# Optimization experiments

Measured on AMD Instinct MI355X. Metric: run time of the kernel, lower is better.

Reference implementation:

```python
import jax, jax.numpy as jnp
import numpy as np

B, L, D, H, DK, DV = 2, 2048, 512, 8, 64, 64
EPS = 1e-6


def setup_inputs() -> dict:
    key = jax.random.key(0)
    ks = jax.random.split(key, 19)
    n = lambda k, s: jax.random.normal(k, s, dtype=jnp.float32)
    inp = {
        "q_r": n(ks[0], (B, L, D)), "q_i": n(ks[1], (B, L, D)),
        "k_r": n(ks[2], (B, L, D)), "k_i": n(ks[3], (B, L, D)),
        "v_r": n(ks[4], (B, L, D)), "v_i": n(ks[5], (B, L, D)),
        "wq_r": n(ks[6], (D, H * DK)) * 0.02, "wq_i": n(ks[7], (D, H * DK)) * 0.02,
        "wk_r": n(ks[8], (D, H * DK)) * 0.02, "wk_i": n(ks[9], (D, H * DK)) * 0.02,
        "wv_r": n(ks[10], (D, H * DV)) * 0.02, "wv_i": n(ks[11], (D, H * DV)) * 0.02,
        "wo_r": n(ks[12], (H * DV, D)) * 0.02, "wo_i": n(ks[13], (H * DV, D)) * 0.02,
        "ln_wr": n(ks[14], (D,)), "ln_wi": n(ks[15], (D,)),
        "ln_br": n(ks[16], (D,)), "ln_bi": n(ks[17], (D,)),
        "mask": jax.random.randint(ks[18], (B, L, L), 0, 2).astype(jnp.int32),
    }
    return inp


def _clinear(xr, xi, wr, wi):
    # complex matmul (xr + i xi) @ (wr + i wi)
    return xr @ wr - xi @ wi, xi @ wr + xr @ wi


def _complex_layernorm(r, i, wr, wi, br, bi, eps=EPS):
    axes = (1, 2)  # normalize over all non-batch dims of [B, L, D]
    r = r - r.mean(axis=axes, keepdims=True)
    i = i - i.mean(axis=axes, keepdims=True)
    Crr = (r * r).mean(axis=axes, keepdims=True) + eps
    Cii = (i * i).mean(axis=axes, keepdims=True) + eps
    Cri = (r * i).mean(axis=axes, keepdims=True)
    s = jnp.sqrt(Crr * Cii - Cri * Cri)
    t = jnp.sqrt(Crr + Cii + 2.0 * s)
    inv_st = 1.0 / (s * t)
    Rrr = (Cii + s) * inv_st
    Rii = (Crr + s) * inv_st
    Rri = -Cri * inv_st
    nr = Rrr * r + Rri * i
    ni = Rii * i + Rri * r
    # affine: complex multiply by (wr + i wi), then add complex bias
    out_r = nr * wr - ni * wi + br
    out_i = nr * wi + ni * wr + bi
    return out_r, out_i


def reference(q_r, q_i, k_r, k_i, v_r, v_i,
              wq_r, wq_i, wk_r, wk_i, wv_r, wv_i, wo_r, wo_i,
              ln_wr, ln_wi, ln_br, ln_bi, mask):
    res_r, res_i = q_r, q_i
    qr, qi = _clinear(q_r, q_i, wq_r, wq_i)
    kr, ki = _clinear(k_r, k_i, wk_r, wk_i)
    vr, vi = _clinear(v_r, v_i, wv_r, wv_i)
    # [B, L, H*Dk] -> [B, H, L, Dk]
    tohead = lambda x, d: x.reshape(B, L, H, d).transpose(0, 2, 1, 3)
    qr, qi = tohead(qr, DK), tohead(qi, DK)
    kr, ki = tohead(kr, DK), tohead(ki, DK)
    vr, vi = tohead(vr, DV), tohead(vi, DV)
    temp = jnp.float32(DK) ** 0.5
    qr, qi = qr / temp, qi / temp
    # complex scores (q @ conj(k)^T): re + i*im
    sr = jnp.einsum('bhqd,bhkd->bhqk', qr, kr) + jnp.einsum('bhqd,bhkd->bhqk', qi, ki)
    si = jnp.einsum('bhqd,bhkd->bhqk', qi, kr) - jnp.einsum('bhqd,bhkd->bhqk', qr, ki)
    a = jnp.sqrt(sr * sr + si * si)  # abs of complex scores
    a = jnp.where(mask[:, None, :, :] == 0, jnp.float32(-1e9), a)
    attn = jax.nn.softmax(a, axis=-1)  # real-valued attention weights
    out_r = jnp.einsum('bhqk,bhkd->bhqd', attn, vr)
    out_i = jnp.einsum('bhqk,bhkd->bhqd', attn, vi)
    # [B, H, L, Dv] -> [B, L, H*Dv]
    out_r = out_r.transpose(0, 2, 1, 3).reshape(B, L, H * DV)
    out_i = out_i.transpose(0, 2, 1, 3).reshape(B, L, H * DV)
    out_r, out_i = _clinear(out_r, out_i, wo_r, wo_i)
    out_r = out_r + res_r
    out_i = out_i + res_i
    out_r, out_i = _complex_layernorm(out_r, out_i, ln_wr, ln_wi, ln_br, ln_bi)
    return out_r, out_i, attn
```

## Files before the change

kernel.cpp:

```cpp
#include <hip/hip_runtime.h>

typedef unsigned short u16;
typedef unsigned int u32;
typedef unsigned long long u64;


typedef __attribute__((ext_vector_type(8))) short bf16x8;
typedef __attribute__((ext_vector_type(4))) float f32x4;
typedef __attribute__((ext_vector_type(4))) u32 u32x4;

__device__ __forceinline__ u16 f2bf(float f) {
  u32 x = __float_as_uint(f);
  return (u16)((x + 0x7FFFu + ((x >> 16) & 1u)) >> 16);
}
__device__ __forceinline__ u32 pk2(float a, float b) {
  return (u32)f2bf(a) | ((u32)f2bf(b) << 16);
}
__device__ __forceinline__ bf16x8 negv(bf16x8 v) {
  u32x4 x = __builtin_bit_cast(u32x4, v);
  x ^= 0x80008000u;
  return __builtin_bit_cast(bf16x8, x);
}


__global__ __launch_bounds__(256) void pack_a3(
    const float* __restrict__ qr, const float* __restrict__ qi,
    const float* __restrict__ kr, const float* __restrict__ ki,
    const float* __restrict__ vr, const float* __restrict__ vi,
    u16* __restrict__ A) {
  int z = blockIdx.y;
  const float* r  = (z == 0) ? qr : (z == 1) ? kr : vr;
  const float* im = (z == 0) ? qi : (z == 1) ? ki : vi;
  int c = blockIdx.x * 256 + threadIdx.x;
  int m = c >> 7;
  int ck = (c & 127) * 8;
  const float* s = (ck < 512) ? (r + (size_t)m * 512 + ck)
                              : (im + (size_t)m * 512 + (ck - 512));
  float4 a = ((const float4*)s)[0];
  float4 b = ((const float4*)s)[1];
  uint4 o;
  o.x = pk2(a.x, a.y); o.y = pk2(a.z, a.w);
  o.z = pk2(b.x, b.y); o.w = pk2(b.z, b.w);
  ((uint4*)(A + (size_t)z * 4194304))[c] = o;
}

__global__ __launch_bounds__(256) void pack_bt(
    const float* __restrict__ wqr, const float* __restrict__ wqi,
    const float* __restrict__ wkr, const float* __restrict__ wki,
    const float* __restrict__ wvr, const float* __restrict__ wvi,
    const float* __restrict__ wor, const float* __restrict__ woi,
    u16* __restrict__ Btb) {
  int z = blockIdx.y;
  const float* wr = (z==0)?wqr:(z==1)?wkr:(z==2)?wvr:wor;
  const float* wi = (z==0)?wqi:(z==1)?wki:(z==2)?wvi:woi;
  u16* Bt = Btb + (size_t)z * 1048576;
  int n0 = (blockIdx.x >> 4) * 64;
  int k0 = (blockIdx.x & 15) * 64;
  __shared__ float tile[64][65];
  int t = threadIdx.x;
  bool nlow = (n0 < 512), klow = (k0 < 512);
  const float* src = nlow ? (klow ? wr : wi) : (klow ? wi : wr);
  float sgn = (nlow && !klow) ? -1.0f : 1.0f;
  int col0 = nlow ? n0 : n0 - 512;
  int kr0 = klow ? k0 : k0 - 512;
  {
    int rr = t >> 2, cc = (t & 3) * 16;
    const float4* s = (const float4*)(src + (size_t)(kr0 + rr) * 512 + col0 + cc);
#pragma unroll
    for (int j = 0; j < 4; ++j) {
      float4 v = s[j];
      tile[rr][cc + j*4 + 0] = v.x; tile[rr][cc + j*4 + 1] = v.y;
      tile[rr][cc + j*4 + 2] = v.z; tile[rr][cc + j*4 + 3] = v.w;
    }
  }
  __syncthreads();
  {
    int nn = t >> 2, kc = (t & 3) * 16;
    u32 w[8];
#pragma unroll
    for (int j = 0; j < 8; ++j)
      w[j] = pk2(sgn * tile[kc + 2*j][nn], sgn * tile[kc + 2*j + 1][nn]);
    uint4* d = (uint4*)(Bt + (size_t)(n0 + nn) * 1024 + k0 + kc);
    d[0] = make_uint4(w[0], w[1], w[2], w[3]);
    d[1] = make_uint4(w[4], w[5], w[6], w[7]);
  }
}

__global__ __launch_bounds__(256) void pack_mask(const int* __restrict__ mask,
                                                 u64* __restrict__ mb) {
  int tid = blockIdx.x * 256 + threadIdx.x;
  u64 bal = __ballot(mask[tid] != 0);
  if ((threadIdx.x & 63) == 0) mb[tid >> 6] = bal;
}

__global__ __launch_bounds__(256) void pack_vt(const u16* __restrict__ Cvm,
                                               u16* __restrict__ vt) {
  int z = blockIdx.y;
  int b = z >> 3, h = z & 7;
  int lt = blockIdx.x >> 1, ct = blockIdx.x & 1;
  int l0 = lt * 64, c0 = ct * 64;
  int n0 = (ct == 0) ? (h * 64) : (512 + h * 64);
  __shared__ u16 tile[64][80];
  int t = threadIdx.x;
  {
    int lr = t >> 2, cc = (t & 3) * 16;
    const uint4* s = (const uint4*)(Cvm + ((size_t)(b * 2048 + l0 + lr)) * 1024 + n0 + cc);
    uint4 v0 = s[0], v1 = s[1];
    *(uint4*)&tile[lr][cc] = v0;
    *(uint4*)&tile[lr][cc + 8] = v1;
  }
  __syncthreads();
  {
    int cr = t >> 2, lc = (t & 3) * 16;
    u32 w[8];
#pragma unroll
    for (int j = 0; j < 8; ++j)
      w[j] = (u32)tile[lc + 2*j][cr] | ((u32)tile[lc + 2*j + 1][cr] << 16);
    uint4* d = (uint4*)(vt + ((size_t)z * 128 + c0 + cr) * 2048 + l0 + lc);
    d[0] = make_uint4(w[0], w[1], w[2], w[3]);
    d[1] = make_uint4(w[4], w[5], w[6], w[7]);
  }
}


__device__ __forceinline__ void stage_bf(const u16* __restrict__ g, int ld,
                                         u16* lds, int t) {
#pragma unroll
  for (int p = 0; p < 4; ++p) {
    int id = p * 256 + t;
    int r = id >> 3, c = id & 7;
    uint4 v = *(const uint4*)(g + (size_t)r * ld + c * 8);
    *(uint4*)(lds + r * 64 + ((c ^ (r & 7)) << 3)) = v;
  }
}
__device__ __forceinline__ void stage64(const u16* __restrict__ g, int ld,
                                        u16* lds, int t) {
#pragma unroll
  for (int p = 0; p < 2; ++p) {
    int id = p * 256 + t;
    int r = id >> 3, c = id & 7;
    uint4 v = *(const uint4*)(g + (size_t)r * ld + c * 8);
    *(uint4*)(lds + r * 64 + ((c ^ (r & 7)) << 3)) = v;
  }
}

__global__ __launch_bounds__(256) void gemm_proj(const u16* __restrict__ Abase,
                                                 const u16* __restrict__ Btbase,
                                                 u16* __restrict__ Cbase) {
  __shared__ u16 lA[128 * 64], lB[128 * 64];
  int t = threadIdx.x, lane = t & 63, wid = t >> 6;
  int c15 = lane & 15, g = lane >> 4, l7 = lane & 7;
  int z = blockIdx.z;
  const u16* A  = Abase  + (size_t)z * 4194304;
  const u16* Bt = Btbase + (size_t)z * 1048576;
  u16* C = Cbase + (size_t)z * 4194304;
  int brow = blockIdx.y * 128, bcol = blockIdx.x * 128;
  float scale = (z == 0) ? 0.125f : 1.0f;
  int sw0 = ((g ^ l7) << 3), sw1 = (((4 | g) ^ l7) << 3);
  int wr0 = (wid >> 1) * 64 + c15, wc0 = (wid & 1) * 64 + c15;
  const u16 *pA0 = lA + wr0 * 64 + sw0, *pA1 = lA + wr0 * 64 + sw1;
  const u16 *pB0 = lB + wc0 * 64 + sw0, *pB1 = lB + wc0 * 64 + sw1;
  f32x4 zero = {0.f, 0.f, 0.f, 0.f};
  f32x4 acc[4][4];
#pragma unroll
  for (int mi = 0; mi < 4; ++mi)
#pragma unroll
    for (int ni = 0; ni < 4; ++ni) acc[mi][ni] = zero;
  for (int kt = 0; kt < 1024; kt += 64) {
    stage_bf(A + (size_t)brow * 1024 + kt, 1024, lA, t);
    stage_bf(Bt + (size_t)bcol * 1024 + kt, 1024, lB, t);
    __syncthreads();
#pragma unroll
    for (int ks = 0; ks < 2; ++ks) {
      const u16* pa = ks ? pA1 : pA0;
      const u16* pb = ks ? pB1 : pB0;
      bf16x8 fa[4], fb[4];
#pragma unroll
      for (int i2 = 0; i2 < 4; ++i2) {
        fa[i2] = *(const bf16x8*)(pa + i2 * 1024);
        fb[i2] = *(const bf16x8*)(pb + i2 * 1024);
      }
#pragma unroll
      for (int mi = 0; mi < 4; ++mi)
#pragma unroll
        for (int ni = 0; ni < 4; ++ni)
          acc[mi][ni] = __builtin_amdgcn_mfma_f32_16x16x32_bf16(
              fa[mi], fb[ni], acc[mi][ni], 0, 0, 0);
    }
    __syncthreads();
  }
  int wrb = (wid >> 1) * 64, wcb = (wid & 1) * 64;
  int rj = g * 4, cj = c15;
#pragma unroll
  for (int mi = 0; mi < 4; ++mi)
#pragma unroll
    for (int ni = 0; ni < 4; ++ni)
#pragma unroll
      for (int j = 0; j < 4; ++j)
        C[(size_t)(brow + wrb + mi * 16 + rj + j) * 1024 +
          (bcol + wcb + ni * 16 + cj)] = f2bf(acc[mi][ni][j] * scale);
}

__global__ __launch_bounds__(256, 3) void fused_attn(
    const u16* __restrict__ Cq, const u16* __restrict__ Ck,
    const u16* __restrict__ vt, const u64* __restrict__ mb,
    float* __restrict__ attn, u16* __restrict__ Ao) {
  __shared__ u16 lKr[64 * 64], lKi[64 * 64], lV[128 * 64], lP[64 * 64];
  int t = threadIdx.x, lane = t & 63, w = t >> 6;
  int c15 = lane & 15, g = lane >> 4, l7 = lane & 7;
  int f = blockIdx.x + (int)gridDim.x * blockIdx.y;
  int wk = (f & 7) * 64 + (f >> 3);
  int strip = wk & 31, z = wk >> 5;
  int b = z >> 3, h = z & 7;
  int q0 = strip * 64;
  int arow = w * 16 + c15;
  int rbase = w * 16 + (g << 2);

  const u16* Qrow = Cq + ((size_t)(b * 2048 + q0 + arow)) * 1024 + h * 64;
  bf16x8 q0r = *(const bf16x8*)(Qrow + g * 8);
  bf16x8 q1r = *(const bf16x8*)(Qrow + 32 + g * 8);
  bf16x8 q0i = *(const bf16x8*)(Qrow + 512 + g * 8);
  bf16x8 q1i = *(const bf16x8*)(Qrow + 544 + g * 8);
  bf16x8 nq0r = negv(q0r), nq1r = negv(q1r);

  int sw0 = ((g ^ l7) << 3), sw1 = (((4 | g) ^ l7) << 3);
  const u16 *pKr0 = lKr + c15 * 64 + sw0, *pKr1 = lKr + c15 * 64 + sw1;
  const u16 *pKi0 = lKi + c15 * 64 + sw0, *pKi1 = lKi + c15 * 64 + sw1;
  const u16 *pV0 = lV + c15 * 64 + sw0, *pV1 = lV + c15 * 64 + sw1;
  const u16 *pP0 = lP + arow * 64 + sw0, *pP1 = lP + arow * 64 + sw1;

  size_t mbase = ((size_t)(b * 2048 + q0 + rbase)) * 32;
  float s[4] = {0.f, 0.f, 0.f, 0.f};
  f32x4 zero = {0.f, 0.f, 0.f, 0.f};
  f32x4 o[8];
#pragma unroll
  for (int ni = 0; ni < 8; ++ni) o[ni] = zero;

  const u16* Kb = Ck + ((size_t)(b * 2048)) * 1024 + h * 64;
  const u16* Vb = vt + (size_t)z * 262144;

  for (int tl = 0; tl < 32; ++tl) {
    int l0 = tl * 64;
    if (tl) __syncthreads();
    stage64(Kb + (size_t)l0 * 1024, 1024, lKr, t);
    stage64(Kb + (size_t)l0 * 1024 + 512, 1024, lKi, t);
    stage_bf(Vb + l0, 2048, lV, t);
    __syncthreads();
    f32x4 sr[4], si[4];
#pragma unroll
    for (int ni = 0; ni < 4; ++ni) { sr[ni] = zero; si[ni] = zero; }
#pragma unroll
    for (int ni = 0; ni < 4; ++ni) {
      bf16x8 g0 = *(const bf16x8*)(pKr0 + ni * 1024);
      bf16x8 g1 = *(const bf16x8*)(pKi0 + ni * 1024);
      sr[ni] = __builtin_amdgcn_mfma_f32_16x16x32_bf16(q0r, g0, sr[ni], 0, 0, 0);
      sr[ni] = __builtin_amdgcn_mfma_f32_16x16x32_bf16(q0i, g1, sr[ni], 0, 0, 0);
      si[ni] = __builtin_amdgcn_mfma_f32_16x16x32_bf16(q0i, g0, si[ni], 0, 0, 0);
      si[ni] = __builtin_amdgcn_mfma_f32_16x16x32_bf16(nq0r, g1, si[ni], 0, 0, 0);
      bf16x8 h0 = *(const bf16x8*)(pKr1 + ni * 1024);
      bf16x8 h1 = *(const bf16x8*)(pKi1 + ni * 1024);
      sr[ni] = __builtin_amdgcn_mfma_f32_16x16x32_bf16(q1r, h0, sr[ni], 0, 0, 0);
      sr[ni] = __builtin_amdgcn_mfma_f32_16x16x32_bf16(q1i, h1, sr[ni], 0, 0, 0);
      si[ni] = __builtin_amdgcn_mfma_f32_16x16x32_bf16(q1i, h0, si[ni], 0, 0, 0);
      si[ni] = __builtin_amdgcn_mfma_f32_16x16x32_bf16(nq1r, h1, si[ni], 0, 0, 0);
    }
    u64 wm[4];
#pragma unroll
    for (int j = 0; j < 4; ++j) wm[j] = mb[mbase + (size_t)j * 32 + tl];
#pragma unroll
    for (int ni = 0; ni < 4; ++ni) {
      int cbit = ni * 16 + c15;
      int pchi = ni * 2 + (c15 >> 3);
#pragma unroll
      for (int j = 0; j < 4; ++j) {
        float n = sr[ni][j] * sr[ni][j] + si[ni][j] * si[ni][j];
        float p = __expf(__builtin_amdgcn_sqrtf(n));
        p = ((wm[j] >> cbit) & 1ull) ? p : 0.0f;
        s[j] += p;
        lP[(rbase + j) * 64 + ((pchi ^ (((g & 1) << 2) + j)) << 3) + l7] = f2bf(p);
      }
    }
    {
      bf16x8 fa0 = *(const bf16x8*)pP0;
      bf16x8 fa1 = *(const bf16x8*)pP1;
#pragma unroll
      for (int ni = 0; ni < 8; ++ni) {
        bf16x8 fb0 = *(const bf16x8*)(pV0 + ni * 1024);
        bf16x8 fb1 = *(const bf16x8*)(pV1 + ni * 1024);
        o[ni] = __builtin_amdgcn_mfma_f32_16x16x32_bf16(fa0, fb0, o[ni], 0, 0, 0);
        o[ni] = __builtin_amdgcn_mfma_f32_16x16x32_bf16(fa1, fb1, o[ni], 0, 0, 0);
      }
    }
  }
  float inv[4];
#pragma unroll
  for (int j = 0; j < 4; ++j) {
    float sj = s[j];
#pragma unroll
    for (int off = 1; off < 16; off <<= 1) sj += __shfl_xor(sj, off);
    inv[j] = 1.0f / sj;
  }
#pragma unroll
  for (int ni = 0; ni < 8; ++ni) {
    int c = ni * 16 + c15;
    int nout = (c < 64) ? (h * 64 + c) : (512 + h * 64 + (c - 64));
#pragma unroll
    for (int j = 0; j < 4; ++j)
      Ao[((size_t)(b * 2048 + q0 + rbase + j)) * 1024 + nout] =
          f2bf(o[ni][j] * inv[j]);
  }
  float* arow_out = attn + ((size_t)z * 2048 + q0 + rbase) * 2048 + c15;
  for (int tl = 0; tl < 32; ++tl) {
    int l0 = tl * 64;
    __syncthreads();
    stage64(Kb + (size_t)l0 * 1024, 1024, lKr, t);
    stage64(Kb + (size_t)l0 * 1024 + 512, 1024, lKi, t);
    __syncthreads();
    f32x4 sr[4], si[4];
#pragma unroll
    for (int ni = 0; ni < 4; ++ni) { sr[ni] = zero; si[ni] = zero; }
#pragma unroll
    for (int ni = 0; ni < 4; ++ni) {
      bf16x8 g0 = *(const bf16x8*)(pKr0 + ni * 1024);
      bf16x8 g1 = *(const bf16x8*)(pKi0 + ni * 1024);
      sr[ni] = __builtin_amdgcn_mfma_f32_16x16x32_bf16(q0r, g0, sr[ni], 0, 0, 0);
      sr[ni] = __builtin_amdgcn_mfma_f32_16x16x32_bf16(q0i, g1, sr[ni], 0, 0, 0);
      si[ni] = __builtin_amdgcn_mfma_f32_16x16x32_bf16(q0i, g0, si[ni], 0, 0, 0);
      si[ni] = __builtin_amdgcn_mfma_f32_16x16x32_bf16(nq0r, g1, si[ni], 0, 0, 0);
      bf16x8 h0 = *(const bf16x8*)(pKr1 + ni * 1024);
      bf16x8 h1 = *(const bf16x8*)(pKi1 + ni * 1024);
      sr[ni] = __builtin_amdgcn_mfma_f32_16x16x32_bf16(q1r, h0, sr[ni], 0, 0, 0);
      sr[ni] = __builtin_amdgcn_mfma_f32_16x16x32_bf16(q1i, h1, sr[ni], 0, 0, 0);
      si[ni] = __builtin_amdgcn_mfma_f32_16x16x32_bf16(q1i, h0, si[ni], 0, 0, 0);
      si[ni] = __builtin_amdgcn_mfma_f32_16x16x32_bf16(nq1r, h1, si[ni], 0, 0, 0);
    }
    u64 wm[4];
#pragma unroll
    for (int j = 0; j < 4; ++j) wm[j] = mb[mbase + (size_t)j * 32 + tl];
    float* outp = arow_out + l0;
#pragma unroll
    for (int ni = 0; ni < 4; ++ni) {
      int cbit = ni * 16 + c15;
#pragma unroll
      for (int j = 0; j < 4; ++j) {
        float n = sr[ni][j] * sr[ni][j] + si[ni][j] * si[ni][j];
        float p = __expf(__builtin_amdgcn_sqrtf(n)) * inv[j];
        p = ((wm[j] >> cbit) & 1ull) ? p : 0.0f;
        outp[(size_t)j * 2048 + ni * 16] = p;
      }
    }
  }
}

__global__ __launch_bounds__(256) void gemm_oproj(
    const u16* __restrict__ A, const u16* __restrict__ Bt,
    const float* __restrict__ resR, const float* __restrict__ resI,
    float* __restrict__ outR, float* __restrict__ outI) {
  __shared__ u16 lA[128 * 64], lB[128 * 64];
  int t = threadIdx.x, lane = t & 63, wid = t >> 6;
  int c15 = lane & 15, g = lane >> 4, l7 = lane & 7;
  int brow = blockIdx.y * 128, bcol = blockIdx.x * 128;
  int sw0 = ((g ^ l7) << 3), sw1 = (((4 | g) ^ l7) << 3);
  int wr0 = (wid >> 1) * 64 + c15, wc0 = (wid & 1) * 64 + c15;
  const u16 *pA0 = lA + wr0 * 64 + sw0, *pA1 = lA + wr0 * 64 + sw1;
  const u16 *pB0 = lB + wc0 * 64 + sw0, *pB1 = lB + wc0 * 64 + sw1;
  f32x4 zero = {0.f, 0.f, 0.f, 0.f};
  f32x4 acc[4][4];
#pragma unroll
  for (int mi = 0; mi < 4; ++mi)
#pragma unroll
    for (int ni = 0; ni < 4; ++ni) acc[mi][ni] = zero;
  for (int kt = 0; kt < 1024; kt += 64) {
    stage_bf(A + (size_t)brow * 1024 + kt, 1024, lA, t);
    stage_bf(Bt + (size_t)bcol * 1024 + kt, 1024, lB, t);
    __syncthreads();
#pragma unroll
    for (int ks = 0; ks < 2; ++ks) {
      const u16* pa = ks ? pA1 : pA0;
      const u16* pb = ks ? pB1 : pB0;
      bf16x8 fa[4], fb[4];
#pragma unroll
      for (int i2 = 0; i2 < 4; ++i2) {
        fa[i2] = *(const bf16x8*)(pa + i2 * 1024);
        fb[i2] = *(const bf16x8*)(pb + i2 * 1024);
      }
#pragma unroll
      for (int mi = 0; mi < 4; ++mi)
#pragma unroll
        for (int ni = 0; ni < 4; ++ni)
          acc[mi][ni] = __builtin_amdgcn_mfma_f32_16x16x32_bf16(
              fa[mi], fb[ni], acc[mi][ni], 0, 0, 0);
    }
    __syncthreads();
  }
  int wrb = (wid >> 1) * 64, wcb = (wid & 1) * 64;
  int rj = g * 4, cj = c15;
#pragma unroll
  for (int mi = 0; mi < 4; ++mi)
#pragma unroll
    for (int ni = 0; ni < 4; ++ni)
#pragma unroll
      for (int j = 0; j < 4; ++j) {
        int row = brow + wrb + mi * 16 + rj + j;
        int col = bcol + wcb + ni * 16 + cj;
        float v = acc[mi][ni][j];
        if (col < 512)
          outR[(size_t)row * 512 + col] = v + resR[(size_t)row * 512 + col];
        else {
          int c2 = col - 512;
          outI[(size_t)row * 512 + c2] = v + resI[(size_t)row * 512 + c2];
        }
      }
}

__global__ void zero_stats(float* __restrict__ stats) {
  if (threadIdx.x < 16) stats[threadIdx.x] = 0.0f;
}

__global__ __launch_bounds__(256) void ln_reduce(const float* __restrict__ outR,
                                                 const float* __restrict__ outI,
                                                 float* __restrict__ stats) {
  int b = blockIdx.y;
  int t = threadIdx.x;
  size_t base = (size_t)b * 1048576 + (size_t)blockIdx.x * 2048;
  float s0 = 0.f, s1 = 0.f, s2 = 0.f, s3 = 0.f, s4 = 0.f;
#pragma unroll
  for (int p = 0; p < 8; ++p) {
    size_t e = base + p * 256 + t;
    float r = outR[e], i = outI[e];
    s0 += r; s1 += i; s2 += r * r; s3 += i * i; s4 += r * i;
  }
#pragma unroll
  for (int off = 32; off; off >>= 1) {
    s0 += __shfl_xor(s0, off); s1 += __shfl_xor(s1, off);
    s2 += __shfl_xor(s2, off); s3 += __shfl_xor(s3, off);
    s4 += __shfl_xor(s4, off);
  }
  __shared__ float red[4][5];
  if ((t & 63) == 0) {
    int w = t >> 6;
    red[w][0] = s0; red[w][1] = s1; red[w][2] = s2; red[w][3] = s3; red[w][4] = s4;
  }
  __syncthreads();
  if (t == 0) {
    float a0 = red[0][0] + red[1][0] + red[2][0] + red[3][0];
    float a1 = red[0][1] + red[1][1] + red[2][1] + red[3][1];
    float a2 = red[0][2] + red[1][2] + red[2][2] + red[3][2];
    float a3 = red[0][3] + red[1][3] + red[2][3] + red[3][3];
    float a4 = red[0][4] + red[1][4] + red[2][4] + red[3][4];
    atomicAdd(&stats[b * 8 + 0], a0);
    atomicAdd(&stats[b * 8 + 1], a1);
    atomicAdd(&stats[b * 8 + 2], a2);
    atomicAdd(&stats[b * 8 + 3], a3);
    atomicAdd(&stats[b * 8 + 4], a4);
  }
}

__global__ __launch_bounds__(256) void ln_apply(
    float* __restrict__ outR, float* __restrict__ outI,
    const float* __restrict__ stats,
    const float* __restrict__ lnwr, const float* __restrict__ lnwi,
    const float* __restrict__ lnbr, const float* __restrict__ lnbi) {
  int b = blockIdx.y;
  const float* st = stats + b * 8;
  float iN = 1.0f / 1048576.0f;
  float mr = st[0] * iN, mi = st[1] * iN;
  float Crr = st[2] * iN - mr * mr + 1e-6f;
  float Cii = st[3] * iN - mi * mi + 1e-6f;
  float Cri = st[4] * iN - mr * mi;
  float s = sqrtf(fmaxf(Crr * Cii - Cri * Cri, 0.f));
  float tt = sqrtf(Crr + Cii + 2.f * s);
  float inv = 1.0f / (s * tt);
  float Rrr = (Cii + s) * inv, Rii = (Crr + s) * inv, Rri = -Cri * inv;
  size_t e = ((size_t)blockIdx.x * 256 + threadIdx.x) * 4;
  size_t idx = (size_t)b * 1048576 + e;
  int d = (int)(e & 511);
  float4 r4 = *(float4*)(outR + idx);
  float4 i4 = *(float4*)(outI + idx);
  float4 wr = *(const float4*)(lnwr + d);
  float4 wi = *(const float4*)(lnwi + d);
  float4 br = *(const float4*)(lnbr + d);
  float4 bi = *(const float4*)(lnbi + d);
  float4 orr, oii;
#pragma unroll
  for (int j = 0; j < 4; ++j) {
    float r = ((&r4.x)[j]) - mr;
    float i = ((&i4.x)[j]) - mi;
    float nr = Rrr * r + Rri * i;
    float ni = Rii * i + Rri * r;
    (&orr.x)[j] = nr * (&wr.x)[j] - ni * (&wi.x)[j] + (&br.x)[j];
    (&oii.x)[j] = nr * (&wi.x)[j] + ni * (&wr.x)[j] + (&bi.x)[j];
  }
  *(float4*)(outR + idx) = orr;
  *(float4*)(outI + idx) = oii;
}

extern "C" void kernel_launch(void* const* d_in, const int* in_sizes, int n_in,
                              void* d_out, int out_size, void* d_ws, size_t ws_size,
                              hipStream_t stream) {
  const float* q_r = (const float*)d_in[0];
  const float* q_i = (const float*)d_in[1];
  const float* k_r = (const float*)d_in[2];
  const float* k_i = (const float*)d_in[3];
  const float* v_r = (const float*)d_in[4];
  const float* v_i = (const float*)d_in[5];
  const float* wq_r = (const float*)d_in[6];
  const float* wq_i = (const float*)d_in[7];
  const float* wk_r = (const float*)d_in[8];
  const float* wk_i = (const float*)d_in[9];
  const float* wv_r = (const float*)d_in[10];
  const float* wv_i = (const float*)d_in[11];
  const float* wo_r = (const float*)d_in[12];
  const float* wo_i = (const float*)d_in[13];
  const float* ln_wr = (const float*)d_in[14];
  const float* ln_wi = (const float*)d_in[15];
  const float* ln_br = (const float*)d_in[16];
  const float* ln_bi = (const float*)d_in[17];
  const int* mask = (const int*)d_in[18];

  float* outR = (float*)d_out;
  float* outI = outR + 2097152;
  float* attn = outR + 4194304;

  char* ws = (char*)d_ws;
  u16* Aq = (u16*)ws;
  u16* Bt = (u16*)(ws + 25165824);
  u16* Cq = (u16*)(ws + 33554432);
  u16* Ck = Cq + 4194304;
  u16* Cv = Cq + 8388608;
  u16* vt = Aq;
  u16* Ao = (u16*)(ws + 58720256);
  u64* mb = (u64*)(ws + 67108864);
  float* stats = (float*)(ws + 69206016);

  pack_a3<<<dim3(2048, 3), 256, 0, stream>>>(q_r, q_i, k_r, k_i, v_r, v_i, Aq);
  pack_bt<<<dim3(256, 4), 256, 0, stream>>>(wq_r, wq_i, wk_r, wk_i, wv_r, wv_i,
                                            wo_r, wo_i, Bt);
  pack_mask<<<dim3(32768), 256, 0, stream>>>(mask, mb);
  zero_stats<<<dim3(1), 64, 0, stream>>>(stats);
  gemm_proj<<<dim3(8, 32, 3), 256, 0, stream>>>(Aq, Bt, Cq);
  pack_vt<<<dim3(64, 16), 256, 0, stream>>>(Cv, vt);
  fused_attn<<<dim3(32, 16), 256, 0, stream>>>(Cq, Ck, vt, mb, attn, Ao);
  gemm_oproj<<<dim3(8, 32), 256, 0, stream>>>(Ao, Bt + 3145728, q_r, q_i, outR, outI);
  ln_reduce<<<dim3(512, 2), 256, 0, stream>>>(outR, outI, stats);
  ln_apply<<<dim3(1024, 2), 256, 0, stream>>>(outR, outI, stats, ln_wr, ln_wi,
                                              ln_br, ln_bi);
}
```

Baseline: 351.2 us.

## Merge prep kernels into one launch and drop LDS staging in attention

The four small preprocessing kernels (mask bit-pack, activation pack, weight transpose-pack, stats zeroing) become one launch that picks its role from the block index, removing launch gaps. The attention kernel no longer stages K and V tiles through shared memory with block-wide barriers. Each wave now loads its MFMA operands straight from global memory and keeps only a private per-wave P buffer in LDS. Barrier waits go away, but K and V are re-fetched once per wave instead of being shared across the block's four waves, which raises global/L2 traffic.

```diff
diff --git a/kernel.cpp b/kernel.cpp
--- a/kernel.cpp
+++ b/kernel.cpp
@@ -22,75 +22,83 @@
   return __builtin_bit_cast(bf16x8, x);
 }
 
-
-__global__ __launch_bounds__(256) void pack_a3(
+__global__ __launch_bounds__(256) void prep(
     const float* __restrict__ qr, const float* __restrict__ qi,
     const float* __restrict__ kr, const float* __restrict__ ki,
     const float* __restrict__ vr, const float* __restrict__ vi,
-    u16* __restrict__ A) {
-  int z = blockIdx.y;
-  const float* r  = (z == 0) ? qr : (z == 1) ? kr : vr;
-  const float* im = (z == 0) ? qi : (z == 1) ? ki : vi;
-  int c = blockIdx.x * 256 + threadIdx.x;
-  int m = c >> 7;
-  int ck = (c & 127) * 8;
-  const float* s = (ck < 512) ? (r + (size_t)m * 512 + ck)
-                              : (im + (size_t)m * 512 + (ck - 512));
-  float4 a = ((const float4*)s)[0];
-  float4 b = ((const float4*)s)[1];
-  uint4 o;
-  o.x = pk2(a.x, a.y); o.y = pk2(a.z, a.w);
-  o.z = pk2(b.x, b.y); o.w = pk2(b.z, b.w);
-  ((uint4*)(A + (size_t)z * 4194304))[c] = o;
-}
-
-__global__ __launch_bounds__(256) void pack_bt(
     const float* __restrict__ wqr, const float* __restrict__ wqi,
     const float* __restrict__ wkr, const float* __restrict__ wki,
     const float* __restrict__ wvr, const float* __restrict__ wvi,
     const float* __restrict__ wor, const float* __restrict__ woi,
-    u16* __restrict__ Btb) {
-  int z = blockIdx.y;
-  const float* wr = (z==0)?wqr:(z==1)?wkr:(z==2)?wvr:wor;
-  const float* wi = (z==0)?wqi:(z==1)?wki:(z==2)?wvi:woi;
-  u16* Bt = Btb + (size_t)z * 1048576;
-  int n0 = (blockIdx.x >> 4) * 64;
-  int k0 = (blockIdx.x & 15) * 64;
+    const int* __restrict__ mask,
+    u16* __restrict__ A, u16* __restrict__ Btb, u64* __restrict__ mb,
+    float* __restrict__ stats) {
   __shared__ float tile[64][65];
+  int bid = blockIdx.x;
   int t = threadIdx.x;
-  bool nlow = (n0 < 512), klow = (k0 < 512);
-  const float* src = nlow ? (klow ? wr : wi) : (klow ? wi : wr);
-  float sgn = (nlow && !klow) ? -1.0f : 1.0f;
-  int col0 = nlow ? n0 : n0 - 512;
-  int kr0 = klow ? k0 : k0 - 512;
-  {
-    int rr = t >> 2, cc = (t & 3) * 16;
-    const float4* s = (const float4*)(src + (size_t)(kr0 + rr) * 512 + col0 + cc);
-#pragma unroll
-    for (int j = 0; j < 4; ++j) {
-      float4 v = s[j];
-      tile[rr][cc + j*4 + 0] = v.x; tile[rr][cc + j*4 + 1] = v.y;
-      tile[rr][cc + j*4 + 2] = v.z; tile[rr][cc + j*4 + 3] = v.w;
-    }
-  }
-  __syncthreads();
-  {
-    int nn = t >> 2, kc = (t & 3) * 16;
-    u32 w[8];
-#pragma unroll
-    for (int j = 0; j < 8; ++j)
-      w[j] = pk2(sgn * tile[kc + 2*j][nn], sgn * tile[kc + 2*j + 1][nn]);
-    uint4* d = (uint4*)(Bt + (size_t)(n0 + nn) * 1024 + k0 + kc);
-    d[0] = make_uint4(w[0], w[1], w[2], w[3]);
-    d[1] = make_uint4(w[4], w[5], w[6], w[7]);
-  }
-}
-
-__global__ __launch_bounds__(256) void pack_mask(const int* __restrict__ mask,
-                                                 u64* __restrict__ mb) {
-  int tid = blockIdx.x * 256 + threadIdx.x;
-  u64 bal = __ballot(mask[tid] != 0);
-  if ((threadIdx.x & 63) == 0) mb[tid >> 6] = bal;
+  if (bid < 32768) {
+    int tid = bid * 256 + t;
+    u64 bal = __ballot(mask[tid] != 0);
+    if ((t & 63) == 0) mb[tid >> 6] = bal;
+    return;
+  }
+  bid -= 32768;
+  if (bid < 6144) {
+    int z = bid >> 11;
+    int bx = bid & 2047;
+    const float* r  = (z == 0) ? qr : (z == 1) ? kr : vr;
+    const float* im = (z == 0) ? qi : (z == 1) ? ki : vi;
+    int c = bx * 256 + t;
+    int m = c >> 7;
+    int ck = (c & 127) * 8;
+    const float* s = (ck < 512) ? (r + (size_t)m * 512 + ck)
+                                : (im + (size_t)m * 512 + (ck - 512));
+    float4 a = ((const float4*)s)[0];
+    float4 b = ((const float4*)s)[1];
+    uint4 o;
+    o.x = pk2(a.x, a.y); o.y = pk2(a.z, a.w);
+    o.z = pk2(b.x, b.y); o.w = pk2(b.z, b.w);
+    ((uint4*)(A + (size_t)z * 4194304))[c] = o;
+    return;
+  }
+  bid -= 6144;
+  if (bid < 1024) {
+    int z = bid >> 8;
+    int bx = bid & 255;
+    const float* wr = (z==0)?wqr:(z==1)?wkr:(z==2)?wvr:wor;
+    const float* wi = (z==0)?wqi:(z==1)?wki:(z==2)?wvi:woi;
+    u16* Bt = Btb + (size_t)z * 1048576;
+    int n0 = (bx >> 4) * 64;
+    int k0 = (bx & 15) * 64;
+    bool nlow = (n0 < 512), klow = (k0 < 512);
+    const float* src = nlow ? (klow ? wr : wi) : (klow ? wi : wr);
+    float sgn = (nlow && !klow) ? -1.0f : 1.0f;
+    int col0 = nlow ? n0 : n0 - 512;
+    int kr0 = klow ? k0 : k0 - 512;
+    {
+      int rr = t >> 2, cc = (t & 3) * 16;
+      const float4* s = (const float4*)(src + (size_t)(kr0 + rr) * 512 + col0 + cc);
+#pragma unroll
+      for (int j = 0; j < 4; ++j) {
+        float4 v = s[j];
+        tile[rr][cc + j*4 + 0] = v.x; tile[rr][cc + j*4 + 1] = v.y;
+        tile[rr][cc + j*4 + 2] = v.z; tile[rr][cc + j*4 + 3] = v.w;
+      }
+    }
+    __syncthreads();
+    {
+      int nn = t >> 2, kc = (t & 3) * 16;
+      u32 w[8];
+#pragma unroll
+      for (int j = 0; j < 8; ++j)
+        w[j] = pk2(sgn * tile[kc + 2*j][nn], sgn * tile[kc + 2*j + 1][nn]);
+      uint4* d = (uint4*)(Bt + (size_t)(n0 + nn) * 1024 + k0 + kc);
+      d[0] = make_uint4(w[0], w[1], w[2], w[3]);
+      d[1] = make_uint4(w[4], w[5], w[6], w[7]);
+    }
+    return;
+  }
+  if (t < 16) stats[t] = 0.0f;
 }
 
 __global__ __launch_bounds__(256) void pack_vt(const u16* __restrict__ Cvm,
@@ -127,16 +135,6 @@
                                          u16* lds, int t) {
 #pragma unroll
   for (int p = 0; p < 4; ++p) {
-    int id = p * 256 + t;
-    int r = id >> 3, c = id & 7;
-    uint4 v = *(const uint4*)(g + (size_t)r * ld + c * 8);
-    *(uint4*)(lds + r * 64 + ((c ^ (r & 7)) << 3)) = v;
-  }
-}
-__device__ __forceinline__ void stage64(const u16* __restrict__ g, int ld,
-                                        u16* lds, int t) {
-#pragma unroll
-  for (int p = 0; p < 2; ++p) {
     int id = p * 256 + t;
     int r = id >> 3, c = id & 7;
     uint4 v = *(const uint4*)(g + (size_t)r * ld + c * 8);
@@ -205,7 +203,7 @@
     const u16* __restrict__ Cq, const u16* __restrict__ Ck,
     const u16* __restrict__ vt, const u64* __restrict__ mb,
     float* __restrict__ attn, u16* __restrict__ Ao) {
-  __shared__ u16 lKr[64 * 64], lKi[64 * 64], lV[128 * 64], lP[64 * 64];
+  __shared__ u16 lP[4][64 * 16];
   int t = threadIdx.x, lane = t & 63, w = t >> 6;
   int c15 = lane & 15, g = lane >> 4, l7 = lane & 7;
   int f = blockIdx.x + (int)gridDim.x * blockIdx.y;
@@ -213,23 +211,22 @@
   int strip = wk & 31, z = wk >> 5;
   int b = z >> 3, h = z & 7;
   int q0 = strip * 64;
-  int arow = w * 16 + c15;
-  int rbase = w * 16 + (g << 2);
-
-  const u16* Qrow = Cq + ((size_t)(b * 2048 + q0 + arow)) * 1024 + h * 64;
+  int arow16 = c15;
+  int rbase16 = g << 2;
+  int qrow = q0 + w * 16;
+
+  const u16* Qrow = Cq + ((size_t)(b * 2048 + qrow + arow16)) * 1024 + h * 64;
   bf16x8 q0r = *(const bf16x8*)(Qrow + g * 8);
   bf16x8 q1r = *(const bf16x8*)(Qrow + 32 + g * 8);
   bf16x8 q0i = *(const bf16x8*)(Qrow + 512 + g * 8);
   bf16x8 q1i = *(const bf16x8*)(Qrow + 544 + g * 8);
   bf16x8 nq0r = negv(q0r), nq1r = negv(q1r);
 
+  u16* myP = lP[w];
   int sw0 = ((g ^ l7) << 3), sw1 = (((4 | g) ^ l7) << 3);
-  const u16 *pKr0 = lKr + c15 * 64 + sw0, *pKr1 = lKr + c15 * 64 + sw1;
-  const u16 *pKi0 = lKi + c15 * 64 + sw0, *pKi1 = lKi + c15 * 64 + sw1;
-  const u16 *pV0 = lV + c15 * 64 + sw0, *pV1 = lV + c15 * 64 + sw1;
-  const u16 *pP0 = lP + arow * 64 + sw0, *pP1 = lP + arow * 64 + sw1;
-
-  size_t mbase = ((size_t)(b * 2048 + q0 + rbase)) * 32;
+  const u16 *pP0 = myP + arow16 * 64 + sw0, *pP1 = myP + arow16 * 64 + sw1;
+
+  size_t mbase = ((size_t)(b * 2048 + qrow + rbase16)) * 32;
   float s[4] = {0.f, 0.f, 0.f, 0.f};
   f32x4 zero = {0.f, 0.f, 0.f, 0.f};
   f32x4 o[8];
@@ -238,35 +235,32 @@
 
   const u16* Kb = Ck + ((size_t)(b * 2048)) * 1024 + h * 64;
   const u16* Vb = vt + (size_t)z * 262144;
+  int g8 = g * 8;
 
   for (int tl = 0; tl < 32; ++tl) {
     int l0 = tl * 64;
-    if (tl) __syncthreads();
-    stage64(Kb + (size_t)l0 * 1024, 1024, lKr, t);
-    stage64(Kb + (size_t)l0 * 1024 + 512, 1024, lKi, t);
-    stage_bf(Vb + l0, 2048, lV, t);
-    __syncthreads();
+    u64 wm[4];
+#pragma unroll
+    for (int j = 0; j < 4; ++j) wm[j] = mb[mbase + (size_t)j * 32 + tl];
     f32x4 sr[4], si[4];
 #pragma unroll
     for (int ni = 0; ni < 4; ++ni) { sr[ni] = zero; si[ni] = zero; }
 #pragma unroll
     for (int ni = 0; ni < 4; ++ni) {
-      bf16x8 g0 = *(const bf16x8*)(pKr0 + ni * 1024);
-      bf16x8 g1 = *(const bf16x8*)(pKi0 + ni * 1024);
+      const u16* kp = Kb + ((size_t)(l0 + ni * 16 + c15) << 10);
+      bf16x8 g0 = *(const bf16x8*)(kp + g8);
+      bf16x8 g1 = *(const bf16x8*)(kp + 512 + g8);
+      bf16x8 h0 = *(const bf16x8*)(kp + 32 + g8);
+      bf16x8 h1 = *(const bf16x8*)(kp + 544 + g8);
       sr[ni] = __builtin_amdgcn_mfma_f32_16x16x32_bf16(q0r, g0, sr[ni], 0, 0, 0);
       sr[ni] = __builtin_amdgcn_mfma_f32_16x16x32_bf16(q0i, g1, sr[ni], 0, 0, 0);
       si[ni] = __builtin_amdgcn_mfma_f32_16x16x32_bf16(q0i, g0, si[ni], 0, 0, 0);
       si[ni] = __builtin_amdgcn_mfma_f32_16x16x32_bf16(nq0r, g1, si[ni], 0, 0, 0);
-      bf16x8 h0 = *(const bf16x8*)(pKr1 + ni * 1024);
-      bf16x8 h1 = *(const bf16x8*)(pKi1 + ni * 1024);
       sr[ni] = __builtin_amdgcn_mfma_f32_16x16x32_bf16(q1r, h0, sr[ni], 0, 0, 0);
       sr[ni] = __builtin_amdgcn_mfma_f32_16x16x32_bf16(q1i, h1, sr[ni], 0, 0, 0);
       si[ni] = __builtin_amdgcn_mfma_f32_16x16x32_bf16(q1i, h0, si[ni], 0, 0, 0);
       si[ni] = __builtin_amdgcn_mfma_f32_16x16x32_bf16(nq1r, h1, si[ni], 0, 0, 0);
     }
-    u64 wm[4];
-#pragma unroll
-    for (int j = 0; j < 4; ++j) wm[j] = mb[mbase + (size_t)j * 32 + tl];
 #pragma unroll
     for (int ni = 0; ni < 4; ++ni) {
       int cbit = ni * 16 + c15;
@@ -277,7 +271,8 @@
         float p = __expf(__builtin_amdgcn_sqrtf(n));
         p = ((wm[j] >> cbit) & 1ull) ? p : 0.0f;
         s[j] += p;
-        lP[(rbase + j) * 64 + ((pchi ^ (((g & 1) << 2) + j)) << 3) + l7] = f2bf(p);
+        myP[(rbase16 + j) * 64 + ((pchi ^ (((g & 1) << 2) + j)) << 3) + l7] =
+            f2bf(p);
       }
     }
     {
@@ -285,8 +280,9 @@
       bf16x8 fa1 = *(const bf16x8*)pP1;
 #pragma unroll
       for (int ni = 0; ni < 8; ++ni) {
-        bf16x8 fb0 = *(const bf16x8*)(pV0 + ni * 1024);
-        bf16x8 fb1 = *(const bf16x8*)(pV1 + ni * 1024);
+        const u16* vp = Vb + ((size_t)(ni * 16 + c15) << 11) + l0;
+        bf16x8 fb0 = *(const bf16x8*)(vp + g8);
+        bf16x8 fb1 = *(const bf16x8*)(vp + 32 + g8);
         o[ni] = __builtin_amdgcn_mfma_f32_16x16x32_bf16(fa0, fb0, o[ni], 0, 0, 0);
         o[ni] = __builtin_amdgcn_mfma_f32_16x16x32_bf16(fa1, fb1, o[ni], 0, 0, 0);
       }
@@ -306,37 +302,34 @@
     int nout = (c < 64) ? (h * 64 + c) : (512 + h * 64 + (c - 64));
 #pragma unroll
     for (int j = 0; j < 4; ++j)
-      Ao[((size_t)(b * 2048 + q0 + rbase + j)) * 1024 + nout] =
+      Ao[((size_t)(b * 2048 + qrow + rbase16 + j)) * 1024 + nout] =
           f2bf(o[ni][j] * inv[j]);
   }
-  float* arow_out = attn + ((size_t)z * 2048 + q0 + rbase) * 2048 + c15;
+  float* arow_out = attn + ((size_t)z * 2048 + qrow + rbase16) * 2048 + c15;
   for (int tl = 0; tl < 32; ++tl) {
     int l0 = tl * 64;
-    __syncthreads();
-    stage64(Kb + (size_t)l0 * 1024, 1024, lKr, t);
-    stage64(Kb + (size_t)l0 * 1024 + 512, 1024, lKi, t);
-    __syncthreads();
+    u64 wm[4];
+#pragma unroll
+    for (int j = 0; j < 4; ++j) wm[j] = mb[mbase + (size_t)j * 32 + tl];
     f32x4 sr[4], si[4];
 #pragma unroll
     for (int ni = 0; ni < 4; ++ni) { sr[ni] = zero; si[ni] = zero; }
 #pragma unroll
     for (int ni = 0; ni < 4; ++ni) {
-      bf16x8 g0 = *(const bf16x8*)(pKr0 + ni * 1024);
-      bf16x8 g1 = *(const bf16x8*)(pKi0 + ni * 1024);
+      const u16* kp = Kb + ((size_t)(l0 + ni * 16 + c15) << 10);
+      bf16x8 g0 = *(const bf16x8*)(kp + g8);
+      bf16x8 g1 = *(const bf16x8*)(kp + 512 + g8);
+      bf16x8 h0 = *(const bf16x8*)(kp + 32 + g8);
+      bf16x8 h1 = *(const bf16x8*)(kp + 544 + g8);
       sr[ni] = __builtin_amdgcn_mfma_f32_16x16x32_bf16(q0r, g0, sr[ni], 0, 0, 0);
       sr[ni] = __builtin_amdgcn_mfma_f32_16x16x32_bf16(q0i, g1, sr[ni], 0, 0, 0);
       si[ni] = __builtin_amdgcn_mfma_f32_16x16x32_bf16(q0i, g0, si[ni], 0, 0, 0);
       si[ni] = __builtin_amdgcn_mfma_f32_16x16x32_bf16(nq0r, g1, si[ni], 0, 0, 0);
-      bf16x8 h0 = *(const bf16x8*)(pKr1 + ni * 1024);
-      bf16x8 h1 = *(const bf16x8*)(pKi1 + ni * 1024);
       sr[ni] = __builtin_amdgcn_mfma_f32_16x16x32_bf16(q1r, h0, sr[ni], 0, 0, 0);
       sr[ni] = __builtin_amdgcn_mfma_f32_16x16x32_bf16(q1i, h1, sr[ni], 0, 0, 0);
       si[ni] = __builtin_amdgcn_mfma_f32_16x16x32_bf16(q1i, h0, si[ni], 0, 0, 0);
       si[ni] = __builtin_amdgcn_mfma_f32_16x16x32_bf16(nq1r, h1, si[ni], 0, 0, 0);
     }
-    u64 wm[4];
-#pragma unroll
-    for (int j = 0; j < 4; ++j) wm[j] = mb[mbase + (size_t)j * 32 + tl];
     float* outp = arow_out + l0;
 #pragma unroll
     for (int ni = 0; ni < 4; ++ni) {
@@ -411,10 +404,6 @@
           outI[(size_t)row * 512 + c2] = v + resI[(size_t)row * 512 + c2];
         }
       }
-}
-
-__global__ void zero_stats(float* __restrict__ stats) {
-  if (threadIdx.x < 16) stats[threadIdx.x] = 0.0f;
 }
 
 __global__ __launch_bounds__(256) void ln_reduce(const float* __restrict__ outR,
@@ -533,11 +522,9 @@
   u64* mb = (u64*)(ws + 67108864);
   float* stats = (float*)(ws + 69206016);
 
-  pack_a3<<<dim3(2048, 3), 256, 0, stream>>>(q_r, q_i, k_r, k_i, v_r, v_i, Aq);
-  pack_bt<<<dim3(256, 4), 256, 0, stream>>>(wq_r, wq_i, wk_r, wk_i, wv_r, wv_i,
-                                            wo_r, wo_i, Bt);
-  pack_mask<<<dim3(32768), 256, 0, stream>>>(mask, mb);
-  zero_stats<<<dim3(1), 64, 0, stream>>>(stats);
+  prep<<<dim3(32768 + 6144 + 1024 + 1), 256, 0, stream>>>(
+      q_r, q_i, k_r, k_i, v_r, v_i, wq_r, wq_i, wk_r, wk_i, wv_r, wv_i,
+      wo_r, wo_i, mask, Aq, Bt, mb, stats);
   gemm_proj<<<dim3(8, 32, 3), 256, 0, stream>>>(Aq, Bt, Cq);
   pack_vt<<<dim3(64, 16), 256, 0, stream>>>(Cv, vt);
   fused_attn<<<dim3(32, 16), 256, 0, stream>>>(Cq, Ck, vt, mb, attn, Ao);
```

Result: slower. 613.5 us (+74.7%).

## Split attention-probability writeback into separate wider kernel and merge prep kernels

Applied to the files above, without the earlier changes.

The fused attention kernel previously recomputed the scores and wrote the full attention matrix in a second 32-tile loop inside the same 512-block launch. That second pass now lives in its own kernel, which splits the key range into four chunks per strip across 2048 blocks and reads the per-row softmax inverse sums from a small workspace buffer. The aim is more parallelism and better occupancy for the write-bound attn output. The four packing and zeroing kernels are also merged into one launch to cut launch overhead, at the cost of an extra kernel boundary and a recomputation of Q loads and scores.

```diff
diff --git a/kernel.cpp b/kernel.cpp
--- a/kernel.cpp
+++ b/kernel.cpp
@@ -22,75 +22,83 @@
   return __builtin_bit_cast(bf16x8, x);
 }
 
-
-__global__ __launch_bounds__(256) void pack_a3(
+__global__ __launch_bounds__(256) void prep(
     const float* __restrict__ qr, const float* __restrict__ qi,
     const float* __restrict__ kr, const float* __restrict__ ki,
     const float* __restrict__ vr, const float* __restrict__ vi,
-    u16* __restrict__ A) {
-  int z = blockIdx.y;
-  const float* r  = (z == 0) ? qr : (z == 1) ? kr : vr;
-  const float* im = (z == 0) ? qi : (z == 1) ? ki : vi;
-  int c = blockIdx.x * 256 + threadIdx.x;
-  int m = c >> 7;
-  int ck = (c & 127) * 8;
-  const float* s = (ck < 512) ? (r + (size_t)m * 512 + ck)
-                              : (im + (size_t)m * 512 + (ck - 512));
-  float4 a = ((const float4*)s)[0];
-  float4 b = ((const float4*)s)[1];
-  uint4 o;
-  o.x = pk2(a.x, a.y); o.y = pk2(a.z, a.w);
-  o.z = pk2(b.x, b.y); o.w = pk2(b.z, b.w);
-  ((uint4*)(A + (size_t)z * 4194304))[c] = o;
-}
-
-__global__ __launch_bounds__(256) void pack_bt(
     const float* __restrict__ wqr, const float* __restrict__ wqi,
     const float* __restrict__ wkr, const float* __restrict__ wki,
     const float* __restrict__ wvr, const float* __restrict__ wvi,
     const float* __restrict__ wor, const float* __restrict__ woi,
-    u16* __restrict__ Btb) {
-  int z = blockIdx.y;
-  const float* wr = (z==0)?wqr:(z==1)?wkr:(z==2)?wvr:wor;
-  const float* wi = (z==0)?wqi:(z==1)?wki:(z==2)?wvi:woi;
-  u16* Bt = Btb + (size_t)z * 1048576;
-  int n0 = (blockIdx.x >> 4) * 64;
-  int k0 = (blockIdx.x & 15) * 64;
+    const int* __restrict__ mask,
+    u16* __restrict__ A, u16* __restrict__ Btb, u64* __restrict__ mb,
+    float* __restrict__ stats) {
   __shared__ float tile[64][65];
+  int bid = blockIdx.x;
   int t = threadIdx.x;
-  bool nlow = (n0 < 512), klow = (k0 < 512);
-  const float* src = nlow ? (klow ? wr : wi) : (klow ? wi : wr);
-  float sgn = (nlow && !klow) ? -1.0f : 1.0f;
-  int col0 = nlow ? n0 : n0 - 512;
-  int kr0 = klow ? k0 : k0 - 512;
-  {
-    int rr = t >> 2, cc = (t & 3) * 16;
-    const float4* s = (const float4*)(src + (size_t)(kr0 + rr) * 512 + col0 + cc);
-#pragma unroll
-    for (int j = 0; j < 4; ++j) {
-      float4 v = s[j];
-      tile[rr][cc + j*4 + 0] = v.x; tile[rr][cc + j*4 + 1] = v.y;
-      tile[rr][cc + j*4 + 2] = v.z; tile[rr][cc + j*4 + 3] = v.w;
-    }
-  }
-  __syncthreads();
-  {
-    int nn = t >> 2, kc = (t & 3) * 16;
-    u32 w[8];
-#pragma unroll
-    for (int j = 0; j < 8; ++j)
-      w[j] = pk2(sgn * tile[kc + 2*j][nn], sgn * tile[kc + 2*j + 1][nn]);
-    uint4* d = (uint4*)(Bt + (size_t)(n0 + nn) * 1024 + k0 + kc);
-    d[0] = make_uint4(w[0], w[1], w[2], w[3]);
-    d[1] = make_uint4(w[4], w[5], w[6], w[7]);
-  }
-}
-
-__global__ __launch_bounds__(256) void pack_mask(const int* __restrict__ mask,
-                                                 u64* __restrict__ mb) {
-  int tid = blockIdx.x * 256 + threadIdx.x;
-  u64 bal = __ballot(mask[tid] != 0);
-  if ((threadIdx.x & 63) == 0) mb[tid >> 6] = bal;
+  if (bid < 32768) {
+    int tid = bid * 256 + t;
+    u64 bal = __ballot(mask[tid] != 0);
+    if ((t & 63) == 0) mb[tid >> 6] = bal;
+    return;
+  }
+  bid -= 32768;
+  if (bid < 6144) {
+    int z = bid >> 11;
+    int bx = bid & 2047;
+    const float* r  = (z == 0) ? qr : (z == 1) ? kr : vr;
+    const float* im = (z == 0) ? qi : (z == 1) ? ki : vi;
+    int c = bx * 256 + t;
+    int m = c >> 7;
+    int ck = (c & 127) * 8;
+    const float* s = (ck < 512) ? (r + (size_t)m * 512 + ck)
+                                : (im + (size_t)m * 512 + (ck - 512));
+    float4 a = ((const float4*)s)[0];
+    float4 b = ((const float4*)s)[1];
+    uint4 o;
+    o.x = pk2(a.x, a.y); o.y = pk2(a.z, a.w);
+    o.z = pk2(b.x, b.y); o.w = pk2(b.z, b.w);
+    ((uint4*)(A + (size_t)z * 4194304))[c] = o;
+    return;
+  }
+  bid -= 6144;
+  if (bid < 1024) {
+    int z = bid >> 8;
+    int bx = bid & 255;
+    const float* wr = (z==0)?wqr:(z==1)?wkr:(z==2)?wvr:wor;
+    const float* wi = (z==0)?wqi:(z==1)?wki:(z==2)?wvi:woi;
+    u16* Bt = Btb + (size_t)z * 1048576;
+    int n0 = (bx >> 4) * 64;
+    int k0 = (bx & 15) * 64;
+    bool nlow = (n0 < 512), klow = (k0 < 512);
+    const float* src = nlow ? (klow ? wr : wi) : (klow ? wi : wr);
+    float sgn = (nlow && !klow) ? -1.0f : 1.0f;
+    int col0 = nlow ? n0 : n0 - 512;
+    int kr0 = klow ? k0 : k0 - 512;
+    {
+      int rr = t >> 2, cc = (t & 3) * 16;
+      const float4* s = (const float4*)(src + (size_t)(kr0 + rr) * 512 + col0 + cc);
+#pragma unroll
+      for (int j = 0; j < 4; ++j) {
+        float4 v = s[j];
+        tile[rr][cc + j*4 + 0] = v.x; tile[rr][cc + j*4 + 1] = v.y;
+        tile[rr][cc + j*4 + 2] = v.z; tile[rr][cc + j*4 + 3] = v.w;
+      }
+    }
+    __syncthreads();
+    {
+      int nn = t >> 2, kc = (t & 3) * 16;
+      u32 w[8];
+#pragma unroll
+      for (int j = 0; j < 8; ++j)
+        w[j] = pk2(sgn * tile[kc + 2*j][nn], sgn * tile[kc + 2*j + 1][nn]);
+      uint4* d = (uint4*)(Bt + (size_t)(n0 + nn) * 1024 + k0 + kc);
+      d[0] = make_uint4(w[0], w[1], w[2], w[3]);
+      d[1] = make_uint4(w[4], w[5], w[6], w[7]);
+    }
+    return;
+  }
+  if (t < 16) stats[t] = 0.0f;
 }
 
 __global__ __launch_bounds__(256) void pack_vt(const u16* __restrict__ Cvm,
@@ -201,10 +209,10 @@
           (bcol + wcb + ni * 16 + cj)] = f2bf(acc[mi][ni][j] * scale);
 }
 
-__global__ __launch_bounds__(256, 3) void fused_attn(
+__global__ __launch_bounds__(256, 3) void fused_p1(
     const u16* __restrict__ Cq, const u16* __restrict__ Ck,
     const u16* __restrict__ vt, const u64* __restrict__ mb,
-    float* __restrict__ attn, u16* __restrict__ Ao) {
+    float* __restrict__ invbuf, u16* __restrict__ Ao) {
   __shared__ u16 lKr[64 * 64], lKi[64 * 64], lV[128 * 64], lP[64 * 64];
   int t = threadIdx.x, lane = t & 63, w = t >> 6;
   int c15 = lane & 15, g = lane >> 4, l7 = lane & 7;
@@ -300,6 +308,11 @@
     for (int off = 1; off < 16; off <<= 1) sj += __shfl_xor(sj, off);
     inv[j] = 1.0f / sj;
   }
+  if (c15 == 0) {
+#pragma unroll
+    for (int j = 0; j < 4; ++j)
+      invbuf[z * 2048 + q0 + rbase + j] = inv[j];
+  }
 #pragma unroll
   for (int ni = 0; ni < 8; ++ni) {
     int c = ni * 16 + c15;
@@ -309,10 +322,48 @@
       Ao[((size_t)(b * 2048 + q0 + rbase + j)) * 1024 + nout] =
           f2bf(o[ni][j] * inv[j]);
   }
+}
+
+__global__ __launch_bounds__(256, 3) void attn_p2(
+    const u16* __restrict__ Cq, const u16* __restrict__ Ck,
+    const u64* __restrict__ mb, const float* __restrict__ invbuf,
+    float* __restrict__ attn) {
+  __shared__ u16 lKr[64 * 64], lKi[64 * 64];
+  int t = threadIdx.x, lane = t & 63, w = t >> 6;
+  int c15 = lane & 15, g = lane >> 4, l7 = lane & 7;
+  int f = blockIdx.x + (int)gridDim.x * blockIdx.y;
+  int wk = (f & 7) * 256 + (f >> 3);
+  int z = wk >> 7;
+  int rem = wk & 127;
+  int strip = rem >> 2, kc = rem & 3;
+  int b = z >> 3, h = z & 7;
+  int q0 = strip * 64;
+  int arow = w * 16 + c15;
+  int rbase = w * 16 + (g << 2);
+
+  const u16* Qrow = Cq + ((size_t)(b * 2048 + q0 + arow)) * 1024 + h * 64;
+  bf16x8 q0r = *(const bf16x8*)(Qrow + g * 8);
+  bf16x8 q1r = *(const bf16x8*)(Qrow + 32 + g * 8);
+  bf16x8 q0i = *(const bf16x8*)(Qrow + 512 + g * 8);
+  bf16x8 q1i = *(const bf16x8*)(Qrow + 544 + g * 8);
+  bf16x8 nq0r = negv(q0r), nq1r = negv(q1r);
+
+  int sw0 = ((g ^ l7) << 3), sw1 = (((4 | g) ^ l7) << 3);
+  const u16 *pKr0 = lKr + c15 * 64 + sw0, *pKr1 = lKr + c15 * 64 + sw1;
+  const u16 *pKi0 = lKi + c15 * 64 + sw0, *pKi1 = lKi + c15 * 64 + sw1;
+
+  size_t mbase = ((size_t)(b * 2048 + q0 + rbase)) * 32;
+  float inv[4];
+#pragma unroll
+  for (int j = 0; j < 4; ++j) inv[j] = invbuf[z * 2048 + q0 + rbase + j];
+  f32x4 zero = {0.f, 0.f, 0.f, 0.f};
+  const u16* Kb = Ck + ((size_t)(b * 2048)) * 1024 + h * 64;
   float* arow_out = attn + ((size_t)z * 2048 + q0 + rbase) * 2048 + c15;
-  for (int tl = 0; tl < 32; ++tl) {
+
+  for (int tt2 = 0; tt2 < 8; ++tt2) {
+    int tl = kc * 8 + tt2;
     int l0 = tl * 64;
-    __syncthreads();
+    if (tt2) __syncthreads();
     stage64(Kb + (size_t)l0 * 1024, 1024, lKr, t);
     stage64(Kb + (size_t)l0 * 1024 + 512, 1024, lKi, t);
     __syncthreads();
@@ -411,10 +462,6 @@
           outI[(size_t)row * 512 + c2] = v + resI[(size_t)row * 512 + c2];
         }
       }
-}
-
-__global__ void zero_stats(float* __restrict__ stats) {
-  if (threadIdx.x < 16) stats[threadIdx.x] = 0.0f;
 }
 
 __global__ __launch_bounds__(256) void ln_reduce(const float* __restrict__ outR,
@@ -532,15 +579,15 @@
   u16* Ao = (u16*)(ws + 58720256);
   u64* mb = (u64*)(ws + 67108864);
   float* stats = (float*)(ws + 69206016);
-
-  pack_a3<<<dim3(2048, 3), 256, 0, stream>>>(q_r, q_i, k_r, k_i, v_r, v_i, Aq);
-  pack_bt<<<dim3(256, 4), 256, 0, stream>>>(wq_r, wq_i, wk_r, wk_i, wv_r, wv_i,
-                                            wo_r, wo_i, Bt);
-  pack_mask<<<dim3(32768), 256, 0, stream>>>(mask, mb);
-  zero_stats<<<dim3(1), 64, 0, stream>>>(stats);
+  float* invbuf = (float*)(ws + 69207040);
+
+  prep<<<dim3(32768 + 6144 + 1024 + 1), 256, 0, stream>>>(
+      q_r, q_i, k_r, k_i, v_r, v_i, wq_r, wq_i, wk_r, wk_i, wv_r, wv_i,
+      wo_r, wo_i, mask, Aq, Bt, mb, stats);
   gemm_proj<<<dim3(8, 32, 3), 256, 0, stream>>>(Aq, Bt, Cq);
   pack_vt<<<dim3(64, 16), 256, 0, stream>>>(Cv, vt);
-  fused_attn<<<dim3(32, 16), 256, 0, stream>>>(Cq, Ck, vt, mb, attn, Ao);
+  fused_p1<<<dim3(32, 16), 256, 0, stream>>>(Cq, Ck, vt, mb, invbuf, Ao);
+  attn_p2<<<dim3(128, 16), 256, 0, stream>>>(Cq, Ck, mb, invbuf, attn);
   gemm_oproj<<<dim3(8, 32), 256, 0, stream>>>(Ao, Bt + 3145728, q_r, q_i, outR, outI);
   ln_reduce<<<dim3(512, 2), 256, 0, stream>>>(outR, outI, stats);
   ln_apply<<<dim3(1024, 2), 256, 0, stream>>>(outR, outI, stats, ln_wr, ln_wi,
```

Measured after the change: 341.5 us. 1.03x faster.
